# Optimization experiments

Hardware: AMD Instinct MI355X
Metric: run time of the kernel (lower is better)

## Reference

```python
import jax, jax.numpy as jnp
import numpy as np

N_NODES = 100000
N_EDGES = 3200000
IN_CH = 128
HID = 128
N_CLASSES = 32
N_GRAPHS = 256


def gcn_conv(x, W, b, src, dst, n_nodes):
    """PyG GCNConv: add self-loops, symmetric deg^-1/2 normalization,
    linear transform, gather-scatter aggregation, bias."""
    xw = x @ W  # [N, out]
    loop = jnp.arange(n_nodes, dtype=src.dtype)
    s = jnp.concatenate([src, loop])  # sources incl. self-loops
    d = jnp.concatenate([dst, loop])  # targets incl. self-loops
    deg = jax.ops.segment_sum(jnp.ones_like(d, dtype=xw.dtype), d,
                              num_segments=n_nodes)
    dinv = jnp.where(deg > 0, jax.lax.rsqrt(deg), 0.0)
    norm = dinv[s] * dinv[d]  # [E+N]
    msgs = xw[s] * norm[:, None]  # gather + scale
    out = jax.ops.segment_sum(msgs, d, num_segments=n_nodes)  # scatter-add
    return out + b


def global_mean_pool(x, batch, n_graphs):
    sums = jax.ops.segment_sum(x, batch, num_segments=n_graphs)
    cnt = jax.ops.segment_sum(jnp.ones((x.shape[0],), x.dtype), batch,
                              num_segments=n_graphs)
    return sums / jnp.maximum(cnt, 1.0)[:, None]


def setup_inputs() -> dict:
    key = jax.random.key(0)
    ks = jax.random.split(key, 9)
    x = jax.random.normal(ks[0], (N_NODES, IN_CH), dtype=jnp.float32)
    edge_index = jax.random.randint(ks[1], (2, N_EDGES), 0, N_NODES, dtype=jnp.int32)
    batch = jnp.sort(jax.random.randint(ks[2], (N_NODES,), 0, N_GRAPHS, dtype=jnp.int32))
    s1 = 1.0 / np.sqrt(IN_CH)
    s2 = 1.0 / np.sqrt(HID)
    W1 = jax.random.uniform(ks[3], (IN_CH, HID), jnp.float32, -s1, s1)
    b1 = jnp.zeros((HID,), jnp.float32)
    W2 = jax.random.uniform(ks[4], (HID, HID), jnp.float32, -s2, s2)
    b2 = jnp.zeros((HID,), jnp.float32)
    Wfc = jax.random.uniform(ks[5], (HID, N_CLASSES), jnp.float32, -s2, s2)
    bfc = jax.random.uniform(ks[6], (N_CLASSES,), jnp.float32, -s2, s2)
    return {"x": x, "edge_index": edge_index, "batch": batch,
            "W1": W1, "b1": b1, "W2": W2, "b2": b2, "Wfc": Wfc, "bfc": bfc}


def reference(x, edge_index, batch, W1, b1, W2, b2, Wfc, bfc):
    src, dst = edge_index[0], edge_index[1]
    h = jax.nn.relu(gcn_conv(x, W1, b1, src, dst, N_NODES))
    h = jax.nn.relu(gcn_conv(h, W2, b2, src, dst, N_NODES))
    g = global_mean_pool(h, batch, N_GRAPHS)  # [G, HID]
    return g @ Wfc + bfc  # [G, N_CLASSES]
```

## Files before the change

### kernel.cpp

```cpp
#include <hip/hip_runtime.h>
#include <hip/hip_bf16.h>
#include <hip/hip_fp16.h>

static constexpr int CH     = 128;
static constexpr int NCLS   = 32;
static constexpr int NGRAPH = 256;

static constexpr int BSHIFT = 8;
static constexpr int BW     = 1 << BSHIFT;
static constexpr int MAXB   = 512;

typedef _Float16 half8 __attribute__((ext_vector_type(8)));
typedef _Float16 half4 __attribute__((ext_vector_type(4)));
typedef float    f32x4 __attribute__((ext_vector_type(4)));
typedef float    f32x2 __attribute__((ext_vector_type(2)));

static constexpr float FP8_SCALE = 64.0f;
static constexpr float FP8_INV   = 1.0f / 64.0f;

__device__ __forceinline__ f32x2 dec8(unsigned short u) {
  return __builtin_amdgcn_cvt_pk_f32_fp8((int)u, false);
}
__device__ __forceinline__ unsigned char enc8(float v) {
  return (unsigned char)(__builtin_amdgcn_cvt_pk_fp8_f32(v, v, 0, false) & 0xFF);
}

__global__ __launch_bounds__(256) void k_init_wt(
    int* __restrict__ gcur, int CAP, int NBUCK, int* __restrict__ xzero,
    const float* __restrict__ W1, const float* __restrict__ W2,
    _Float16* __restrict__ WhT1, _Float16* __restrict__ WhT2) {
  int t = threadIdx.x;
  if (blockIdx.x == 0) {
    for (int i = t; i < NBUCK; i += 256) gcur[i] = i * CAP;
    if (t < 32) xzero[t] = 0;
    return;
  }
  int i = (blockIdx.x - 1) * 256 + t;
  const float* W = (i < CH * CH) ? W1 : W2;
  _Float16* T   = (i < CH * CH) ? WhT1 : WhT2;
  int j = i & (CH * CH - 1);
  int k = j >> 7, n = j & 127;
  T[n * CH + k] = (_Float16)W[j];
}

__global__ __launch_bounds__(1024) void k_scatter(
    const int* __restrict__ src, const int* __restrict__ dst,
    int* __restrict__ gcur, int* __restrict__ ebuf, int E) {
  __shared__ int bcnt[MAXB];
  __shared__ int bbase[MAXB];
  int t = threadIdx.x;
  if (t < MAXB) bcnt[t] = 0;
  __syncthreads();
  int base = blockIdx.x * 8192;
  int s_[8], d_[8], r_[8];
  #pragma unroll
  for (int j = 0; j < 8; ++j) {
    int i = base + j * 1024 + t;
    if (i < E) {
      s_[j] = src[i];
      d_[j] = dst[i];
      r_[j] = atomicAdd(&bcnt[d_[j] >> BSHIFT], 1);
    }
  }
  __syncthreads();
  if (t < MAXB && bcnt[t]) bbase[t] = atomicAdd(&gcur[t], bcnt[t]);
  __syncthreads();
  #pragma unroll
  for (int j = 0; j < 8; ++j) {
    int i = base + j * 1024 + t;
    if (i < E) {
      int b = d_[j] >> BSHIFT;
      int p = ((d_[j] & (BW - 1)) << 17) | s_[j];
      ebuf[bbase[b] + r_[j]] = p;
    }
  }
}

__global__ __launch_bounds__(1024) void k_build(
    const int* __restrict__ ebuf, const int* __restrict__ gcur,
    int* __restrict__ offs, int* __restrict__ oend,
    float* __restrict__ dinv, int* __restrict__ csr, int N, int CAP) {
  __shared__ int sdeg[BW];
  __shared__ int sscan[BW];
  int b = blockIdx.x;
  int t = threadIdx.x;
  int lo = b << BSHIFT;
  int e0 = b * CAP;
  int e1 = gcur[b];

  if (t < BW) sdeg[t] = 0;
  __syncthreads();
  for (int e = e0 + t; e < e1; e += 1024)
    atomicAdd(&sdeg[ebuf[e] >> 17], 1);
  __syncthreads();
  if (t < BW) sscan[t] = (sdeg[t] + 3) & ~3;
  __syncthreads();
  for (int st = 1; st < BW; st <<= 1) {
    int v = (t < BW && t >= st) ? sscan[t - st] : 0;
    __syncthreads();
    if (t < BW) sscan[t] += v;
    __syncthreads();
  }
  if (t < BW) {
    int deg  = sdeg[t];
    int pdeg = (deg + 3) & ~3;
    int ex = b * CAP + sscan[t] - pdeg;
    int n = lo + t;
    if (n < N) {
      offs[n] = ex;
      oend[n] = ex + deg;
      dinv[n] = 1.0f / sqrtf((float)(deg + 1));
      for (int q = deg; q < pdeg; ++q) csr[ex + q] = N;
    }
    sscan[t] = ex;
  }
  __syncthreads();
  for (int e = e0 + t; e < e1; e += 1024) {
    int p = ebuf[e];
    int pos = atomicAdd(&sscan[p >> 17], 1);
    csr[pos] = p & 0x1FFFF;
  }
}

__device__ __forceinline__ void stage_w(const _Float16* __restrict__ WhT,
                                        _Float16 (*Ws)[136], int tid) {
  #pragma unroll
  for (int l = 0; l < 8; ++l) {
    int idx = tid + l * 256;
    int n = idx >> 4, k8 = (idx & 15) << 3;
    *(half8*)&Ws[n][k8] = *(const half8*)(WhT + n * CH + k8);
  }
}

__device__ __forceinline__ void gemm_core64(
    const _Float16 (*As)[136], const _Float16 (*Ws)[136],
    const float* __restrict__ dinv, unsigned char* __restrict__ C,
    int row0, int M, int tid) {
  int lane = tid & 63, wave = tid >> 6;
  int quad = lane >> 4, sub = lane & 15;
  int m0 = wave * 16;

  f32x4 acc[8];
  #pragma unroll
  for (int j = 0; j < 8; ++j) acc[j] = (f32x4){0.f, 0.f, 0.f, 0.f};

  #pragma unroll
  for (int kc = 0; kc < 4; ++kc) {
    int ko = kc * 32 + quad * 8;
    half8 a = *(const half8*)&As[m0 + sub][ko];
    #pragma unroll
    for (int nt = 0; nt < 8; ++nt) {
      half8 b = *(const half8*)&Ws[nt * 16 + sub][ko];
      acc[nt] = __builtin_amdgcn_mfma_f32_16x16x32_f16(a, b, acc[nt], 0, 0, 0);
    }
  }
  #pragma unroll
  for (int r = 0; r < 4; ++r) {
    int row = row0 + m0 + quad * 4 + r;
    if (row < M) {
      float d = dinv[row] * FP8_SCALE;
      #pragma unroll
      for (int nt = 0; nt < 8; ++nt)
        C[(size_t)row * CH + nt * 16 + sub] = enc8(acc[nt][r] * d);
    }
  }
}

__global__ __launch_bounds__(256) void k_gemm_f32(
    const float* __restrict__ A, const _Float16* __restrict__ WhT,
    const float* __restrict__ dinv, unsigned char* __restrict__ C, int M) {
  __shared__ _Float16 As[64][136];
  __shared__ _Float16 Ws[128][136];
  int tid = threadIdx.x;
  int row0 = blockIdx.x * 64;
  #pragma unroll
  for (int l = 0; l < 8; ++l) {
    int idx = tid + l * 256;
    int r = idx >> 5, c4 = (idx & 31) << 2;
    int rr = row0 + r; if (rr >= M) rr = M - 1;
    float4 v = *(const float4*)(A + (size_t)rr * CH + c4);
    half4 hv = { (_Float16)v.x, (_Float16)v.y, (_Float16)v.z, (_Float16)v.w };
    *(half4*)&As[r][c4] = hv;
  }
  stage_w(WhT, Ws, tid);
  __syncthreads();
  gemm_core64(As, Ws, dinv, C, row0, M, tid);
}

__global__ __launch_bounds__(256) void k_gemm_f16(
    const _Float16* __restrict__ A, const _Float16* __restrict__ WhT,
    const float* __restrict__ dinv, unsigned char* __restrict__ C, int M) {
  __shared__ _Float16 As[64][136];
  __shared__ _Float16 Ws[128][136];
  int tid = threadIdx.x;
  int row0 = blockIdx.x * 64;
  #pragma unroll
  for (int l = 0; l < 4; ++l) {
    int idx = tid + l * 256;
    int r = idx >> 4, c8 = (idx & 15) << 3;
    int rr = row0 + r; if (rr >= M) rr = M - 1;
    *(half8*)&As[r][c8] = *(const half8*)(A + (size_t)rr * CH + c8);
  }
  stage_w(WhT, Ws, tid);
  __syncthreads();
  gemm_core64(As, Ws, dinv, C, row0, M, tid);
}

__global__ __launch_bounds__(256) void k_agg(
    const unsigned char* __restrict__ xs, const int* __restrict__ csr,
    const int* __restrict__ offs, const int* __restrict__ oend,
    const float* __restrict__ dinv, const float* __restrict__ bias,
    __half* __restrict__ out, int N) {
  int wid0  = blockIdx.x * 4 + (threadIdx.x >> 6);
  int lane  = threadIdx.x & 63;
  int wstep = gridDim.x * 4;
  unsigned int lane2 = (unsigned int)lane << 1;
  float2 bxy = *(const float2*)(bias + 2 * lane);

  auto g = [&](int s) -> unsigned short {
    return *(const unsigned short*)(xs + (((unsigned int)s << 7) | lane2));
  };

  for (int wid = wid0; wid * 2 < N; wid += wstep) {
    int nA = wid * 2, nB = nA + 1;
    bool hasB = (nB < N);

    int eA = offs[nA];
    int cA = (oend[nA] - eA + 3) >> 2;
    int eB = hasB ? offs[nB] : eA;
    int cB = hasB ? ((oend[nB] - eB + 3) >> 2) : 0;

    f32x2 aA0 = dec8(g(nA));
    f32x2 aA1 = {0.f, 0.f};
    f32x2 aB0 = {0.f, 0.f}, aB1 = {0.f, 0.f};
    if (hasB) aB0 = dec8(g(nB));

    if (cA >= 2 && cB >= 2) {
      int4 ca0 = *(const int4*)(csr + eA);
      int4 ca1 = *(const int4*)(csr + eA + 4);
      int4 cb0 = *(const int4*)(csr + eB);
      int4 cb1 = *(const int4*)(csr + eB + 4);
      do {
        unsigned short uA0 = g(ca0.x), uA1 = g(ca0.y), uA2 = g(ca0.z), uA3 = g(ca0.w);
        unsigned short uA4 = g(ca1.x), uA5 = g(ca1.y), uA6 = g(ca1.z), uA7 = g(ca1.w);
        unsigned short uB0 = g(cb0.x), uB1 = g(cb0.y), uB2 = g(cb0.z), uB3 = g(cb0.w);
        unsigned short uB4 = g(cb1.x), uB5 = g(cb1.y), uB6 = g(cb1.z), uB7 = g(cb1.w);
        eA += 8; eB += 8; cA -= 2; cB -= 2;
        int4 na0 = *(const int4*)(csr + eA);
        int4 na1 = *(const int4*)(csr + eA + 4);
        int4 nb0 = *(const int4*)(csr + eB);
        int4 nb1 = *(const int4*)(csr + eB + 4);
        aA0 += dec8(uA0); aA1 += dec8(uA1); aA0 += dec8(uA2); aA1 += dec8(uA3);
        aA0 += dec8(uA4); aA1 += dec8(uA5); aA0 += dec8(uA6); aA1 += dec8(uA7);
        aB0 += dec8(uB0); aB1 += dec8(uB1); aB0 += dec8(uB2); aB1 += dec8(uB3);
        aB0 += dec8(uB4); aB1 += dec8(uB5); aB0 += dec8(uB6); aB1 += dec8(uB7);
        ca0 = na0; ca1 = na1; cb0 = nb0; cb1 = nb1;
      } while (cA >= 2 && cB >= 2);
    }

    auto drain = [&](int e, int c, f32x2& a0, f32x2& a1) {
      while (c >= 2) {
        int4 q0 = *(const int4*)(csr + e);
        int4 q1 = *(const int4*)(csr + e + 4);
        unsigned short u0 = g(q0.x), u1 = g(q0.y), u2 = g(q0.z), u3 = g(q0.w);
        unsigned short u4 = g(q1.x), u5 = g(q1.y), u6 = g(q1.z), u7 = g(q1.w);
        a0 += dec8(u0); a1 += dec8(u1); a0 += dec8(u2); a1 += dec8(u3);
        a0 += dec8(u4); a1 += dec8(u5); a0 += dec8(u6); a1 += dec8(u7);
        e += 8; c -= 2;
      }
      if (c > 0) {
        int4 q0 = *(const int4*)(csr + e);
        unsigned short u0 = g(q0.x), u1 = g(q0.y), u2 = g(q0.z), u3 = g(q0.w);
        a0 += dec8(u0); a1 += dec8(u1); a0 += dec8(u2); a1 += dec8(u3);
      }
    };
    drain(eA, cA, aA0, aA1);
    if (hasB) drain(eB, cB, aB0, aB1);

    {
      f32x2 s = aA0 + aA1;
      float dn = dinv[nA] * FP8_INV;
      float rx = fmaf(s[0], dn, bxy.x);
      float ry = fmaf(s[1], dn, bxy.y);
      ((__half2*)out)[(size_t)nA * 64 + lane] =
          __floats2half2_rn(fmaxf(rx, 0.f), fmaxf(ry, 0.f));
    }
    if (hasB) {
      f32x2 s = aB0 + aB1;
      float dn = dinv[nB] * FP8_INV;
      float rx = fmaf(s[0], dn, bxy.x);
      float ry = fmaf(s[1], dn, bxy.y);
      ((__half2*)out)[(size_t)nB * 64 + lane] =
          __floats2half2_rn(fmaxf(rx, 0.f), fmaxf(ry, 0.f));
    }
  }
}

__global__ __launch_bounds__(128) void k_pool(
    const __half* __restrict__ h, const int* __restrict__ batch,
    float* __restrict__ gsum, int* __restrict__ gstart,
    int* __restrict__ gend, int N) {
  int ch = threadIdx.x;
  int n0 = blockIdx.x * 128;
  int n1 = n0 + 128; if (n1 > N) n1 = N;
  if (n0 >= N) return;
  for (int n = n0 + ch; n < n1; n += 128) {
    int g = batch[n];
    if (n == 0 || batch[n - 1] != g) gstart[g] = n;
    if (n == N - 1 || batch[n + 1] != g) gend[g] = n + 1;
  }
  float acc = 0.f;
  int curg = batch[n0];
  for (int n = n0; n < n1; ++n) {
    int g = batch[n];
    if (g != curg) {
      atomicAdd(&gsum[curg * CH + ch], acc);
      acc = 0.f; curg = g;
    }
    acc += __half2float(h[(size_t)n * CH + ch]);
  }
  atomicAdd(&gsum[curg * CH + ch], acc);
}

__global__ __launch_bounds__(64) void k_fc(
    const float* __restrict__ gsum, const int* __restrict__ gstart,
    const int* __restrict__ gend, const float* __restrict__ Wfc,
    const float* __restrict__ bfc, float* __restrict__ outp) {
  int g = blockIdx.x;
  int j = threadIdx.x;
  if (j >= NCLS) return;
  int cnt = gend[g] - gstart[g];
  float invc = 1.0f / fmaxf((float)cnt, 1.0f);
  float acc = 0.0f;
  for (int c = 0; c < CH; ++c)
    acc = fmaf(gsum[g * CH + c], Wfc[c * NCLS + j], acc);
  outp[g * NCLS + j] = fmaf(acc, invc, bfc[j]);
}

extern "C" void kernel_launch(void* const* d_in, const int* in_sizes, int n_in,
                              void* d_out, int out_size, void* d_ws, size_t ws_size,
                              hipStream_t stream) {
  const float* x    = (const float*)d_in[0];
  const int*   ei   = (const int*)d_in[1];
  const int*   batch= (const int*)d_in[2];
  const float* W1   = (const float*)d_in[3];
  const float* b1   = (const float*)d_in[4];
  const float* W2   = (const float*)d_in[5];
  const float* b2   = (const float*)d_in[6];
  const float* Wfc  = (const float*)d_in[7];
  const float* bfc  = (const float*)d_in[8];
  float* outp = (float*)d_out;

  const int N = in_sizes[0] / CH;
  const int E = in_sizes[1] / 2;
  const int* src = ei;
  const int* dst = ei + E;
  const int NBUCK = (N + BW - 1) >> BSHIFT;
  int CAP = (E / NBUCK) + (E / NBUCK) / 8 + 1280;
  CAP = (CAP + 3) & ~3;

  char* w = (char*)d_ws;
  size_t o = 0;
  auto carve = [&](size_t bytes) -> void* {
    o = (o + 255) & ~(size_t)255;
    void* p = w + o;
    o += bytes;
    return p;
  };
  float*    gsum   = (float*)   carve((size_t)NGRAPH * CH * 4);
  int*      gstart = (int*)     carve((size_t)NGRAPH * 4);
  int*      gend   = (int*)     carve((size_t)NGRAPH * 4);
  size_t zbytes = o;
  int*      offs   = (int*)     carve((size_t)N * 4);
  int*      oendb  = (int*)     carve((size_t)N * 4);
  int*      gcur   = (int*)     carve(MAXB * 4);
  int*      csr    = (int*)     carve((size_t)NBUCK * CAP * 4);
  float*    dinv   = (float*)   carve((size_t)N * 4);
  _Float16* WhT1   = (_Float16*)carve((size_t)CH * CH * 2);
  _Float16* WhT2   = (_Float16*)carve((size_t)CH * CH * 2);
  unsigned char* xsbuf = (unsigned char*)carve((size_t)(N + 1) * CH);
  __half*   hbuf   = (__half*)  carve((size_t)N * CH * 2);
  (void)ws_size;

  int* ebuf = (int*)hbuf;

  (void)hipMemsetAsync(gsum, 0, zbytes, stream);

  const int GB64 = (N + 63) / 64;
  const int GB   = (N + 127) / 128;
  int AB = (N + 7) / 8;
  if (AB > 2048) AB = 2048;

  k_init_wt<<<129, 256, 0, stream>>>(gcur, CAP, NBUCK,
                                     (int*)(xsbuf + (size_t)N * CH),
                                     W1, W2, WhT1, WhT2);
  k_scatter<<<(E + 8191) / 8192, 1024, 0, stream>>>(src, dst, gcur, ebuf, E);
  k_build  <<<NBUCK, 1024, 0, stream>>>(ebuf, gcur, offs, oendb, dinv, csr, N, CAP);

  k_gemm_f32<<<GB64, 256, 0, stream>>>(x, WhT1, dinv, xsbuf, N);
  k_agg<<<AB, 256, 0, stream>>>(xsbuf, csr, offs, oendb, dinv, b1, hbuf, N);
  k_gemm_f16<<<GB64, 256, 0, stream>>>((const _Float16*)hbuf, WhT2, dinv, xsbuf, N);
  k_agg<<<AB, 256, 0, stream>>>(xsbuf, csr, offs, oendb, dinv, b2, hbuf, N);

  k_pool<<<GB, 128, 0, stream>>>(hbuf, batch, gsum, gstart, gend, N);
  k_fc<<<NGRAPH, 64, 0, stream>>>(gsum, gstart, gend, Wfc, bfc, outp);
  (void)out_size; (void)n_in;
}
```

Baseline: 350.0 us.

## Split FP8 feature table into two 64-channel halves aggregated in separate passes

The GEMM epilogue now writes the FP8 node-feature table as two planar halves of 64 channels each (64 bytes per node per half), and each aggregation layer runs as two launches, one per half. The aim is to halve the gathered working set per pass (about 6.4 MB per half) so it fits better in L2/LLC during random-neighbour gathers. The cost is reading the CSR indices twice, doing byte-granularity gathers with one channel per lane, and extra kernel launches.

Result: slower. 475.7 us (+35.9%).

```diff
diff --git a/kernel.cpp b/kernel.cpp
--- a/kernel.cpp
+++ b/kernel.cpp
@@ -18,21 +18,26 @@
 static constexpr float FP8_SCALE = 64.0f;
 static constexpr float FP8_INV   = 1.0f / 64.0f;
 
-__device__ __forceinline__ f32x2 dec8(unsigned short u) {
-  return __builtin_amdgcn_cvt_pk_f32_fp8((int)u, false);
+__device__ __forceinline__ float dec8_lo(unsigned char u) {
+  f32x2 t = __builtin_amdgcn_cvt_pk_f32_fp8((int)u, false);
+  return t[0];
 }
 __device__ __forceinline__ unsigned char enc8(float v) {
   return (unsigned char)(__builtin_amdgcn_cvt_pk_fp8_f32(v, v, 0, false) & 0xFF);
 }
 
 __global__ __launch_bounds__(256) void k_init_wt(
-    int* __restrict__ gcur, int CAP, int NBUCK, int* __restrict__ xzero,
+    int* __restrict__ gcur, int CAP, int NBUCK,
+    int* __restrict__ xzero, int zstride_words,
     const float* __restrict__ W1, const float* __restrict__ W2,
     _Float16* __restrict__ WhT1, _Float16* __restrict__ WhT2) {
   int t = threadIdx.x;
   if (blockIdx.x == 0) {
     for (int i = t; i < NBUCK; i += 256) gcur[i] = i * CAP;
-    if (t < 32) xzero[t] = 0;
+    if (t < 16) {
+      xzero[t] = 0;
+      xzero[zstride_words + t] = 0;
+    }
     return;
   }
   int i = (blockIdx.x - 1) * 256 + t;
@@ -139,6 +144,7 @@
   int lane = tid & 63, wave = tid >> 6;
   int quad = lane >> 4, sub = lane & 15;
   int m0 = wave * 16;
+  size_t NP1 = (size_t)M + 1;
 
   f32x4 acc[8];
   #pragma unroll
@@ -160,8 +166,11 @@
     if (row < M) {
       float d = dinv[row] * FP8_SCALE;
       #pragma unroll
-      for (int nt = 0; nt < 8; ++nt)
-        C[(size_t)row * CH + nt * 16 + sub] = enc8(acc[nt][r] * d);
+      for (int nt = 0; nt < 8; ++nt) {
+        int ch = nt * 16 + sub;
+        size_t cidx = ((size_t)(ch >> 6) * NP1 + row) * 64 + (ch & 63);
+        C[cidx] = enc8(acc[nt][r] * d);
+      }
     }
   }
 }
@@ -207,18 +216,17 @@
 }
 
 __global__ __launch_bounds__(256) void k_agg(
-    const unsigned char* __restrict__ xs, const int* __restrict__ csr,
+    const unsigned char* __restrict__ xsp, const int* __restrict__ csr,
     const int* __restrict__ offs, const int* __restrict__ oend,
-    const float* __restrict__ dinv, const float* __restrict__ bias,
-    __half* __restrict__ out, int N) {
+    const float* __restrict__ dinv, const float* __restrict__ biasp,
+    __half* __restrict__ outp, int N) {
   int wid0  = blockIdx.x * 4 + (threadIdx.x >> 6);
   int lane  = threadIdx.x & 63;
   int wstep = gridDim.x * 4;
-  unsigned int lane2 = (unsigned int)lane << 1;
-  float2 bxy = *(const float2*)(bias + 2 * lane);
-
-  auto g = [&](int s) -> unsigned short {
-    return *(const unsigned short*)(xs + (((unsigned int)s << 7) | lane2));
+  float bb = biasp[lane];
+
+  auto g = [&](int s) -> unsigned char {
+    return xsp[((unsigned int)s << 6) | (unsigned int)lane];
   };
 
   for (int wid = wid0; wid * 2 < N; wid += wstep) {
@@ -230,10 +238,9 @@
     int eB = hasB ? offs[nB] : eA;
     int cB = hasB ? ((oend[nB] - eB + 3) >> 2) : 0;
 
-    f32x2 aA0 = dec8(g(nA));
-    f32x2 aA1 = {0.f, 0.f};
-    f32x2 aB0 = {0.f, 0.f}, aB1 = {0.f, 0.f};
-    if (hasB) aB0 = dec8(g(nB));
+    float aA0 = dec8_lo(g(nA)), aA1 = 0.f;
+    float aB0 = 0.f, aB1 = 0.f;
+    if (hasB) aB0 = dec8_lo(g(nB));
 
     if (cA >= 2 && cB >= 2) {
       int4 ca0 = *(const int4*)(csr + eA);
@@ -241,57 +248,55 @@
       int4 cb0 = *(const int4*)(csr + eB);
       int4 cb1 = *(const int4*)(csr + eB + 4);
       do {
-        unsigned short uA0 = g(ca0.x), uA1 = g(ca0.y), uA2 = g(ca0.z), uA3 = g(ca0.w);
-        unsigned short uA4 = g(ca1.x), uA5 = g(ca1.y), uA6 = g(ca1.z), uA7 = g(ca1.w);
-        unsigned short uB0 = g(cb0.x), uB1 = g(cb0.y), uB2 = g(cb0.z), uB3 = g(cb0.w);
-        unsigned short uB4 = g(cb1.x), uB5 = g(cb1.y), uB6 = g(cb1.z), uB7 = g(cb1.w);
+        unsigned char uA0 = g(ca0.x), uA1 = g(ca0.y), uA2 = g(ca0.z), uA3 = g(ca0.w);
+        unsigned char uA4 = g(ca1.x), uA5 = g(ca1.y), uA6 = g(ca1.z), uA7 = g(ca1.w);
+        unsigned char uB0 = g(cb0.x), uB1 = g(cb0.y), uB2 = g(cb0.z), uB3 = g(cb0.w);
+        unsigned char uB4 = g(cb1.x), uB5 = g(cb1.y), uB6 = g(cb1.z), uB7 = g(cb1.w);
         eA += 8; eB += 8; cA -= 2; cB -= 2;
         int4 na0 = *(const int4*)(csr + eA);
         int4 na1 = *(const int4*)(csr + eA + 4);
         int4 nb0 = *(const int4*)(csr + eB);
         int4 nb1 = *(const int4*)(csr + eB + 4);
-        aA0 += dec8(uA0); aA1 += dec8(uA1); aA0 += dec8(uA2); aA1 += dec8(uA3);
-        aA0 += dec8(uA4); aA1 += dec8(uA5); aA0 += dec8(uA6); aA1 += dec8(uA7);
-        aB0 += dec8(uB0); aB1 += dec8(uB1); aB0 += dec8(uB2); aB1 += dec8(uB3);
-        aB0 += dec8(uB4); aB1 += dec8(uB5); aB0 += dec8(uB6); aB1 += dec8(uB7);
+        aA0 += dec8_lo(uA0); aA1 += dec8_lo(uA1);
+        aA0 += dec8_lo(uA2); aA1 += dec8_lo(uA3);
+        aA0 += dec8_lo(uA4); aA1 += dec8_lo(uA5);
+        aA0 += dec8_lo(uA6); aA1 += dec8_lo(uA7);
+        aB0 += dec8_lo(uB0); aB1 += dec8_lo(uB1);
+        aB0 += dec8_lo(uB2); aB1 += dec8_lo(uB3);
+        aB0 += dec8_lo(uB4); aB1 += dec8_lo(uB5);
+        aB0 += dec8_lo(uB6); aB1 += dec8_lo(uB7);
         ca0 = na0; ca1 = na1; cb0 = nb0; cb1 = nb1;
       } while (cA >= 2 && cB >= 2);
     }
 
-    auto drain = [&](int e, int c, f32x2& a0, f32x2& a1) {
+    auto drain = [&](int e, int c, float& a0, float& a1) {
       while (c >= 2) {
         int4 q0 = *(const int4*)(csr + e);
         int4 q1 = *(const int4*)(csr + e + 4);
-        unsigned short u0 = g(q0.x), u1 = g(q0.y), u2 = g(q0.z), u3 = g(q0.w);
-        unsigned short u4 = g(q1.x), u5 = g(q1.y), u6 = g(q1.z), u7 = g(q1.w);
-        a0 += dec8(u0); a1 += dec8(u1); a0 += dec8(u2); a1 += dec8(u3);
-        a0 += dec8(u4); a1 += dec8(u5); a0 += dec8(u6); a1 += dec8(u7);
+        unsigned char u0 = g(q0.x), u1 = g(q0.y), u2 = g(q0.z), u3 = g(q0.w);
+        unsigned char u4 = g(q1.x), u5 = g(q1.y), u6 = g(q1.z), u7 = g(q1.w);
+        a0 += dec8_lo(u0); a1 += dec8_lo(u1); a0 += dec8_lo(u2); a1 += dec8_lo(u3);
+        a0 += dec8_lo(u4); a1 += dec8_lo(u5); a0 += dec8_lo(u6); a1 += dec8_lo(u7);
         e += 8; c -= 2;
       }
       if (c > 0) {
         int4 q0 = *(const int4*)(csr + e);
-        unsigned short u0 = g(q0.x), u1 = g(q0.y), u2 = g(q0.z), u3 = g(q0.w);
-        a0 += dec8(u0); a1 += dec8(u1); a0 += dec8(u2); a1 += dec8(u3);
+        unsigned char u0 = g(q0.x), u1 = g(q0.y), u2 = g(q0.z), u3 = g(q0.w);
+        a0 += dec8_lo(u0); a1 += dec8_lo(u1); a0 += dec8_lo(u2); a1 += dec8_lo(u3);
       }
     };
     drain(eA, cA, aA0, aA1);
     if (hasB) drain(eB, cB, aB0, aB1);
 
     {
-      f32x2 s = aA0 + aA1;
       float dn = dinv[nA] * FP8_INV;
-      float rx = fmaf(s[0], dn, bxy.x);
-      float ry = fmaf(s[1], dn, bxy.y);
-      ((__half2*)out)[(size_t)nA * 64 + lane] =
-          __floats2half2_rn(fmaxf(rx, 0.f), fmaxf(ry, 0.f));
+      float r = fmaf(aA0 + aA1, dn, bb);
+      outp[(size_t)nA * CH + lane] = __float2half(fmaxf(r, 0.f));
     }
     if (hasB) {
-      f32x2 s = aB0 + aB1;
       float dn = dinv[nB] * FP8_INV;
-      float rx = fmaf(s[0], dn, bxy.x);
-      float ry = fmaf(s[1], dn, bxy.y);
-      ((__half2*)out)[(size_t)nB * 64 + lane] =
-          __floats2half2_rn(fmaxf(rx, 0.f), fmaxf(ry, 0.f));
+      float r = fmaf(aB0 + aB1, dn, bb);
+      outp[(size_t)nB * CH + lane] = __float2half(fmaxf(r, 0.f));
     }
   }
 }
@@ -378,9 +383,11 @@
   float*    dinv   = (float*)   carve((size_t)N * 4);
   _Float16* WhT1   = (_Float16*)carve((size_t)CH * CH * 2);
   _Float16* WhT2   = (_Float16*)carve((size_t)CH * CH * 2);
-  unsigned char* xsbuf = (unsigned char*)carve((size_t)(N + 1) * CH);
+  unsigned char* xsbuf = (unsigned char*)carve((size_t)2 * (N + 1) * 64);
   __half*   hbuf   = (__half*)  carve((size_t)N * CH * 2);
   (void)ws_size;
+
+  const size_t HALF = (size_t)(N + 1) * 64;
 
   int* ebuf = (int*)hbuf;
 
@@ -392,15 +399,18 @@
   if (AB > 2048) AB = 2048;
 
   k_init_wt<<<129, 256, 0, stream>>>(gcur, CAP, NBUCK,
-                                     (int*)(xsbuf + (size_t)N * CH),
+                                     (int*)(xsbuf + (size_t)N * 64),
+                                     (int)(HALF / 4),
                                      W1, W2, WhT1, WhT2);
   k_scatter<<<(E + 8191) / 8192, 1024, 0, stream>>>(src, dst, gcur, ebuf, E);
   k_build  <<<NBUCK, 1024, 0, stream>>>(ebuf, gcur, offs, oendb, dinv, csr, N, CAP);
 
   k_gemm_f32<<<GB64, 256, 0, stream>>>(x, WhT1, dinv, xsbuf, N);
-  k_agg<<<AB, 256, 0, stream>>>(xsbuf, csr, offs, oendb, dinv, b1, hbuf, N);
+  k_agg<<<AB, 256, 0, stream>>>(xsbuf,        csr, offs, oendb, dinv, b1,      hbuf,      N);
+  k_agg<<<AB, 256, 0, stream>>>(xsbuf + HALF, csr, offs, oendb, dinv, b1 + 64, hbuf + 64, N);
   k_gemm_f16<<<GB64, 256, 0, stream>>>((const _Float16*)hbuf, WhT2, dinv, xsbuf, N);
-  k_agg<<<AB, 256, 0, stream>>>(xsbuf, csr, offs, oendb, dinv, b2, hbuf, N);
+  k_agg<<<AB, 256, 0, stream>>>(xsbuf,        csr, offs, oendb, dinv, b2,      hbuf,      N);
+  k_agg<<<AB, 256, 0, stream>>>(xsbuf + HALF, csr, offs, oendb, dinv, b2 + 64, hbuf + 64, N);
 
   k_pool<<<GB, 128, 0, stream>>>(hbuf, batch, gsum, gstart, gend, N);
   k_fc<<<NGRAPH, 64, 0, stream>>>(gsum, gstart, gend, Wfc, bfc, outp);
```
